# Optimization experiments

Hardware: AMD Instinct MI355X
Metric: run time of the kernel (lower is better)

The kernel has to match this reference:

```python
import jax, jax.numpy as jnp
import numpy as np

B, D, N, C = 4096, 2048, 8, 1024  # batch, in_features, ncomponents, per-component out channels


def setup_inputs() -> dict:
    key = jax.random.key(0)
    k1, k2, k3, k4 = jax.random.split(key, 4)
    scale_w = 1.0 / np.sqrt(D)
    return {
        "x": jax.random.normal(k1, (B, D), dtype=jnp.float32),
        "W": jax.random.normal(k2, (N, C, D), dtype=jnp.float32) * scale_w,
        "b": jax.random.normal(k3, (N, C), dtype=jnp.float32) * scale_w,
        "Wg_w": jax.random.normal(k4, (D, 1), dtype=jnp.float32) * scale_w,
        "Wg_b": jnp.zeros((1,), dtype=jnp.float32),
    }


def reference(x, W, b, Wg_w, Wg_b):
    n = W.shape[0]
    # scalar gate per sample: g in [0, ncomponents]
    g = n * 0.5 * (1.0 + jnp.tanh(x @ Wg_w + Wg_b))            # [B, 1]
    k = jnp.floor(g)                                            # [B, 1]
    idx = jnp.arange(n, dtype=x.dtype)[None, :]                 # [1, N]
    M_hard = (idx <= k).astype(x.dtype)                        # monotonic prefix mask [B, N]
    # straight-through estimator: forward = hard mask, grad wrt g = sum over components
    M = jax.lax.stop_gradient(M_hard - g) + g                   # [B, N]
    # L1 normalize (torch fn.normalize p=1, eps=1e-12)
    G = M / jnp.maximum(jnp.sum(jnp.abs(M), axis=1, keepdims=True), 1e-12)
    # all component outputs; unselected components have G==0 so they contribute the
    # same zeros the original pads with (equal-width components, out = N*C)
    Y = jnp.einsum('bd,ncd->bnc', x, W) + b                     # [B, N, C]
    E = (G[:, :, None] * Y).reshape(x.shape[0], -1)             # [B, N*C]
    return E, G
```

## Files before the change

### kernel.cpp

```cpp
#include <hip/hip_runtime.h>
#include <hip/hip_bf16.h>

#define BATCH 4096
#define DK    2048
#define NCOMP 8
#define NC    8192
#define NT    (DK / 64)

typedef unsigned int u32;
typedef unsigned short u16;
typedef short bf16x8 __attribute__((ext_vector_type(8)));
typedef float f32x4 __attribute__((ext_vector_type(4)));

__device__ __forceinline__ u16 f2bf(float f) {
    union { float f; u32 u; } v; v.f = f;
    u32 r = v.u + 0x7fffu + ((v.u >> 16) & 1u);
    return (u16)(r >> 16);
}

__global__ void cvtW_kernel(const float* __restrict__ in, u16* __restrict__ out) {
    int i = blockIdx.x * blockDim.x + threadIdx.x;
    float4 a = ((const float4*)in)[i];
    ushort4 o = { f2bf(a.x), f2bf(a.y), f2bf(a.z), f2bf(a.w) };
    ((ushort4*)out)[i] = o;
}

__global__ __launch_bounds__(256)
void xgate_kernel(const float* __restrict__ x, const float* __restrict__ wg,
                  const float* __restrict__ wgb, u16* __restrict__ xb,
                  float* __restrict__ G) {
    int row = blockIdx.x;
    int t = threadIdx.x;
    const float4* xr = (const float4*)(x + (size_t)row * DK);
    const float4* wr = (const float4*)wg;
    float4 a = xr[t], b = xr[t + 256];
    float4 wa = wr[t], wb = wr[t + 256];
    float s = a.x*wa.x + a.y*wa.y + a.z*wa.z + a.w*wa.w
            + b.x*wb.x + b.y*wb.y + b.z*wb.z + b.w*wb.w;
    ushort4 o1 = { f2bf(a.x), f2bf(a.y), f2bf(a.z), f2bf(a.w) };
    ushort4 o2 = { f2bf(b.x), f2bf(b.y), f2bf(b.z), f2bf(b.w) };
    ushort4* xo = (ushort4*)(xb + (size_t)row * DK);
    xo[t] = o1;
    xo[t + 256] = o2;
    __shared__ float red[4];
#pragma unroll
    for (int off = 32; off; off >>= 1) s += __shfl_xor(s, off, 64);
    if ((t & 63) == 0) red[t >> 6] = s;
    __syncthreads();
    if (t == 0) {
        float sum = (red[0] + red[1]) + (red[2] + red[3]);
        float g = 0.5f * (float)NCOMP * (1.0f + tanhf(sum + wgb[0]));
        float k = floorf(g);
        float mh[NCOMP]; float den = 0.f;
#pragma unroll
        for (int n = 0; n < NCOMP; ++n) {
            float m = ((float)n <= k) ? 1.0f : 0.0f;
            m = (m - g) + g;
            mh[n] = m; den += fabsf(m);
        }
        den = fmaxf(den, 1e-12f);
#pragma unroll
        for (int n = 0; n < NCOMP; ++n) G[(size_t)row * NCOMP + n] = mh[n] / den;
    }
}

__device__ __forceinline__ void stage_half(const u16* __restrict__ gbase,
                                           u16* __restrict__ ldsHalf, int tid) {
#pragma unroll
    for (int i = 0; i < 2; ++i) {
        int c = tid + i * 512;
        int row = c >> 3;
        int slot = (c & 7) ^ (row & 7);
        const u16* src = gbase + (size_t)row * DK + slot * 8;
        u16* dst = ldsHalf + (size_t)(c >> 6) * 512;
        __builtin_amdgcn_global_load_lds((const __attribute__((address_space(1))) u32*)src,
                                         (__attribute__((address_space(3))) u32*)dst, 16, 0, 0);
    }
}

__device__ __forceinline__ bf16x8 frag(const u16* __restrict__ h, int lrow, int slot) {
    return *(const bf16x8*)(h + lrow * 64 + ((slot ^ (lrow & 7)) << 3));
}

#define PH_MID()  do { __builtin_amdgcn_s_barrier(); \
    asm volatile("s_waitcnt lgkmcnt(0)" ::: "memory"); \
    __builtin_amdgcn_sched_barrier(0); \
    __builtin_amdgcn_s_setprio(1); } while (0)
#define PH_END()  do { __builtin_amdgcn_s_setprio(0); \
    __builtin_amdgcn_s_barrier(); } while (0)

__global__ __launch_bounds__(512, 2)
void gemm_kernel(const u16* __restrict__ A, const u16* __restrict__ Bw,
                 const float* __restrict__ bias, const float* __restrict__ Gtab,
                 float* __restrict__ E) {
    __shared__ u16 lds[2][2][2][128 * 64];
    int tid = threadIdx.x;
    int l = tid & 63;
    int w = tid >> 6;
    int wr = w >> 2, wc = w & 3;
    int r16 = l & 15, kg = l >> 4;

    int bid = blockIdx.x;
    int swz = (bid & 7) * 64 + (bid >> 3);
    int brow = (swz >> 5) * 256;
    int bcol = (swz & 31) * 256;

    f32x4 acc[8][4] = {};

    const u16* gA = A + (size_t)brow * DK;
    const u16* gB = Bw + (size_t)bcol * DK;

    stage_half(gA,              lds[0][0][0], tid);
    stage_half(gA + 128 * DK,   lds[0][0][1], tid);
    stage_half(gB,              lds[0][1][0], tid);
    stage_half(gB + 128 * DK,   lds[0][1][1], tid);
    asm volatile("s_waitcnt vmcnt(0)" ::: "memory");
    __builtin_amdgcn_s_barrier();

    for (int t = 0; t < NT; ++t) {
        int buf = t & 1, nb = buf ^ 1;
        const u16* Ah = lds[buf][0][wr];
        const u16* Bh = lds[buf][1][wc >> 1];
        int brB = (wc & 1) * 64;
        int koff = (t + 1) * 64;
        bool pf = (t + 1) < NT;

        bf16x8 aF[4][2], bF[2][2];
#pragma unroll
        for (int j = 0; j < 4; ++j)
#pragma unroll
            for (int kk = 0; kk < 2; ++kk)
                aF[j][kk] = frag(Ah, j * 16 + r16, kk * 4 + kg);
#pragma unroll
        for (int jn = 0; jn < 2; ++jn)
#pragma unroll
            for (int kk = 0; kk < 2; ++kk)
                bF[jn][kk] = frag(Bh, brB + jn * 16 + r16, kk * 4 + kg);
        if (pf) {
            stage_half(gA + koff,            lds[nb][0][0], tid);
            stage_half(gA + 128 * DK + koff, lds[nb][0][1], tid);
        }
        PH_MID();
#pragma unroll
        for (int j = 0; j < 4; ++j)
#pragma unroll
            for (int jn = 0; jn < 2; ++jn)
#pragma unroll
                for (int kk = 0; kk < 2; ++kk)
                    acc[j][jn] = __builtin_amdgcn_mfma_f32_16x16x32_bf16(aF[j][kk], bF[jn][kk], acc[j][jn], 0, 0, 0);
        PH_END();

        bf16x8 bG[2][2];
#pragma unroll
        for (int jn = 0; jn < 2; ++jn)
#pragma unroll
            for (int kk = 0; kk < 2; ++kk)
                bG[jn][kk] = frag(Bh, brB + 32 + jn * 16 + r16, kk * 4 + kg);
        if (pf) {
            stage_half(gB + koff,            lds[nb][1][0], tid);
            stage_half(gB + 128 * DK + koff, lds[nb][1][1], tid);
        }
        PH_MID();
#pragma unroll
        for (int j = 0; j < 4; ++j)
#pragma unroll
            for (int jn = 0; jn < 2; ++jn)
#pragma unroll
                for (int kk = 0; kk < 2; ++kk)
                    acc[j][2 + jn] = __builtin_amdgcn_mfma_f32_16x16x32_bf16(aF[j][kk], bG[jn][kk], acc[j][2 + jn], 0, 0, 0);
        PH_END();

        bf16x8 aG[4][2];
#pragma unroll
        for (int j = 0; j < 4; ++j)
#pragma unroll
            for (int kk = 0; kk < 2; ++kk)
                aG[j][kk] = frag(Ah, 64 + j * 16 + r16, kk * 4 + kg);
        PH_MID();
#pragma unroll
        for (int j = 0; j < 4; ++j)
#pragma unroll
            for (int jn = 0; jn < 2; ++jn)
#pragma unroll
                for (int kk = 0; kk < 2; ++kk)
                    acc[4 + j][2 + jn] = __builtin_amdgcn_mfma_f32_16x16x32_bf16(aG[j][kk], bG[jn][kk], acc[4 + j][2 + jn], 0, 0, 0);
        PH_END();

#pragma unroll
        for (int jn = 0; jn < 2; ++jn)
#pragma unroll
            for (int kk = 0; kk < 2; ++kk)
                bF[jn][kk] = frag(Bh, brB + jn * 16 + r16, kk * 4 + kg);
        PH_MID();
#pragma unroll
        for (int j = 0; j < 4; ++j)
#pragma unroll
            for (int jn = 0; jn < 2; ++jn)
#pragma unroll
                for (int kk = 0; kk < 2; ++kk)
                    acc[4 + j][jn] = __builtin_amdgcn_mfma_f32_16x16x32_bf16(aG[j][kk], bF[jn][kk], acc[4 + j][jn], 0, 0, 0);
        __builtin_amdgcn_s_setprio(0);
        if (pf) asm volatile("s_waitcnt vmcnt(0)" ::: "memory");
        __builtin_amdgcn_s_barrier();
    }

    int ncomp = (bcol + wc * 64) >> 10;
    int rbase = brow + wr * 128;
    int cbase = bcol + wc * 64;
    float bs[4];
#pragma unroll
    for (int ni = 0; ni < 4; ++ni) bs[ni] = bias[cbase + ni * 16 + r16];
#pragma unroll
    for (int mi = 0; mi < 8; ++mi)
#pragma unroll
        for (int r = 0; r < 4; ++r) {
            int row = rbase + mi * 16 + kg * 4 + r;
            float gv = Gtab[(size_t)row * NCOMP + ncomp];
            float* Erow = E + (size_t)row * NC + cbase;
#pragma unroll
            for (int ni = 0; ni < 4; ++ni)
                Erow[ni * 16 + r16] = gv * (acc[mi][ni][r] + bs[ni]);
        }
}

extern "C" void kernel_launch(void* const* d_in, const int* in_sizes, int n_in,
                              void* d_out, int out_size, void* d_ws, size_t ws_size,
                              hipStream_t stream) {
    const float* x   = (const float*)d_in[0];
    const float* W   = (const float*)d_in[1];
    const float* b   = (const float*)d_in[2];
    const float* wgw = (const float*)d_in[3];
    const float* wgb = (const float*)d_in[4];
    float* E = (float*)d_out;
    float* G = E + (size_t)BATCH * NC;

    u16* xb = (u16*)d_ws;
    u16* Wb = xb + (size_t)BATCH * DK;

    cvtW_kernel<<<NC * DK / 4 / 256, 256, 0, stream>>>(W, Wb);
    xgate_kernel<<<BATCH, 256, 0, stream>>>(x, wgw, wgb, xb, G);
    gemm_kernel<<<(BATCH / 256) * (NC / 256), 512, 0, stream>>>(xb, Wb, b, G, E);
}
```

Baseline: 327.9 us.

## Deepen GEMM prefetch to two tiles ahead with partial vmcnt waits

Global-to-LDS staging is reorganized so the loads for tile t+2 go into the buffer of the current tile as soon as each half has been consumed. The half-tile for t+1 is issued early in the iteration. The end-of-iteration wait becomes vmcnt(6) instead of vmcnt(0), which keeps about three stage_half loads in flight across iterations to hide global memory latency. The redundant reload of the bF fragments from LDS in the last phase is dropped, and the registers are reused instead. The risks are correctness hazards in the buffer reuse ordering and more register pressure from keeping aG, bF and bG live.

```diff
diff --git a/kernel.cpp b/kernel.cpp
--- a/kernel.cpp
+++ b/kernel.cpp
@@ -110,22 +110,28 @@
     const u16* gA = A + (size_t)brow * DK;
     const u16* gB = Bw + (size_t)bcol * DK;
 
-    stage_half(gA,              lds[0][0][0], tid);
-    stage_half(gA + 128 * DK,   lds[0][0][1], tid);
-    stage_half(gB,              lds[0][1][0], tid);
-    stage_half(gB + 128 * DK,   lds[0][1][1], tid);
-    asm volatile("s_waitcnt vmcnt(0)" ::: "memory");
+    stage_half(gA,                 lds[0][0][0], tid);
+    stage_half(gA + 128 * DK,      lds[0][0][1], tid);
+    stage_half(gB,                 lds[0][1][0], tid);
+    stage_half(gB + 128 * DK,      lds[0][1][1], tid);
+    stage_half(gB + 64,            lds[1][1][0], tid);
+    stage_half(gB + 128 * DK + 64, lds[1][1][1], tid);
+    stage_half(gA + 64,            lds[1][0][0], tid);
+    asm volatile("s_waitcnt vmcnt(6)" ::: "memory");
     __builtin_amdgcn_s_barrier();
 
     for (int t = 0; t < NT; ++t) {
-        int buf = t & 1, nb = buf ^ 1;
-        const u16* Ah = lds[buf][0][wr];
-        const u16* Bh = lds[buf][1][wc >> 1];
+        int p = t & 1;
+        const u16* Ah = lds[p][0][wr];
+        const u16* Bh = lds[p][1][wc >> 1];
         int brB = (wc & 1) * 64;
-        int koff = (t + 1) * 64;
-        bool pf = (t + 1) < NT;
-
-        bf16x8 aF[4][2], bF[2][2];
+        bool pf1 = (t + 1) < NT;
+        bool pf2 = (t + 2) < NT;
+        int koff1 = (t + 1) * 64;
+        int koff2 = (t + 2) * 64;
+
+        bf16x8 aF[4][2], aG[4][2], bF[2][2], bG[2][2];
+
 #pragma unroll
         for (int j = 0; j < 4; ++j)
 #pragma unroll
@@ -136,10 +142,7 @@
 #pragma unroll
             for (int kk = 0; kk < 2; ++kk)
                 bF[jn][kk] = frag(Bh, brB + jn * 16 + r16, kk * 4 + kg);
-        if (pf) {
-            stage_half(gA + koff,            lds[nb][0][0], tid);
-            stage_half(gA + 128 * DK + koff, lds[nb][0][1], tid);
-        }
+        if (pf1) stage_half(gA + 128 * DK + koff1, lds[p ^ 1][0][1], tid);
         PH_MID();
 #pragma unroll
         for (int j = 0; j < 4; ++j)
@@ -150,16 +153,11 @@
                     acc[j][jn] = __builtin_amdgcn_mfma_f32_16x16x32_bf16(aF[j][kk], bF[jn][kk], acc[j][jn], 0, 0, 0);
         PH_END();
 
-        bf16x8 bG[2][2];
 #pragma unroll
         for (int jn = 0; jn < 2; ++jn)
 #pragma unroll
             for (int kk = 0; kk < 2; ++kk)
                 bG[jn][kk] = frag(Bh, brB + 32 + jn * 16 + r16, kk * 4 + kg);
-        if (pf) {
-            stage_half(gB + koff,            lds[nb][1][0], tid);
-            stage_half(gB + 128 * DK + koff, lds[nb][1][1], tid);
-        }
         PH_MID();
 #pragma unroll
         for (int j = 0; j < 4; ++j)
@@ -170,12 +168,12 @@
                     acc[j][2 + jn] = __builtin_amdgcn_mfma_f32_16x16x32_bf16(aF[j][kk], bG[jn][kk], acc[j][2 + jn], 0, 0, 0);
         PH_END();
 
-        bf16x8 aG[4][2];
 #pragma unroll
         for (int j = 0; j < 4; ++j)
 #pragma unroll
             for (int kk = 0; kk < 2; ++kk)
                 aG[j][kk] = frag(Ah, 64 + j * 16 + r16, kk * 4 + kg);
+        if (pf2) stage_half(gB + koff2, lds[p][1][0], tid);
         PH_MID();
 #pragma unroll
         for (int j = 0; j < 4; ++j)
@@ -186,11 +184,10 @@
                     acc[4 + j][2 + jn] = __builtin_amdgcn_mfma_f32_16x16x32_bf16(aG[j][kk], bG[jn][kk], acc[4 + j][2 + jn], 0, 0, 0);
         PH_END();
 
-#pragma unroll
-        for (int jn = 0; jn < 2; ++jn)
-#pragma unroll
-            for (int kk = 0; kk < 2; ++kk)
-                bF[jn][kk] = frag(Bh, brB + jn * 16 + r16, kk * 4 + kg);
+        if (pf2) {
+            stage_half(gB + 128 * DK + koff2, lds[p][1][1], tid);
+            stage_half(gA + koff2,            lds[p][0][0], tid);
+        }
         PH_MID();
 #pragma unroll
         for (int j = 0; j < 4; ++j)
@@ -200,8 +197,9 @@
                 for (int kk = 0; kk < 2; ++kk)
                     acc[4 + j][jn] = __builtin_amdgcn_mfma_f32_16x16x32_bf16(aG[j][kk], bF[jn][kk], acc[4 + j][jn], 0, 0, 0);
         __builtin_amdgcn_s_setprio(0);
-        if (pf) asm volatile("s_waitcnt vmcnt(0)" ::: "memory");
-        __builtin_amdgcn_s_barrier();
+        if (pf2)      asm volatile("s_waitcnt vmcnt(6)" ::: "memory");
+        else if (pf1) asm volatile("s_waitcnt vmcnt(0)" ::: "memory");
+        if (pf1) __builtin_amdgcn_s_barrier();
     }
 
     int ncomp = (bcol + wc * 64) >> 10;
```

New measurement: 326.8 us. About the same (-0.3%).
